# Optimization experiments

Measured on AMD Instinct MI355X. Metric: run time of the kernel, lower is better.

## Reference

```python
import jax, jax.numpy as jnp
import numpy as np
import math

B, S, E, H = 1, 4096, 1024, 16
D = E // H  # head_dim = 64

def setup_inputs() -> dict:
    key = jax.random.key(0)
    kx, kq, kk, kv, ko = jax.random.split(key, 5)
    sc = 1.0 / math.sqrt(E)
    return {
        "x": jax.random.normal(kx, (B, S, E), dtype=jnp.float32),
        "Wq": jax.random.normal(kq, (E, E), dtype=jnp.float32) * sc,
        "Wk": jax.random.normal(kk, (E, E), dtype=jnp.float32) * sc,
        "Wv": jax.random.normal(kv, (E, E), dtype=jnp.float32) * sc,
        "Wo": jax.random.normal(ko, (E, E), dtype=jnp.float32) * sc,
    }

def reference(x, Wq, Wk, Wv, Wo):
    b, s, _ = x.shape
    # nn.Linear(no bias): x @ W.T ; then split heads -> [b, H, s, D]
    def heads(w):
        return (x @ w.T).reshape(b, s, H, D).transpose(0, 2, 1, 3)
    q, k, v = heads(Wq), heads(Wk), heads(Wv)
    scale = 1.0 / math.sqrt(D)
    logits = jnp.einsum('bhqd,bhkd->bhqk', q, k) * scale  # [b,H,s,s]
    causal = jnp.tril(jnp.ones((s, s), dtype=bool))
    logits = jnp.where(causal, logits, -jnp.inf)
    attn = jax.nn.softmax(logits, axis=-1)
    out = jnp.einsum('bhqk,bhkd->bhqd', attn, v)  # [b,H,s,D]
    out = out.transpose(0, 2, 1, 3).reshape(b, s, E)
    return out @ Wo.T
```

## Files before the change

### kernel.cpp

```cpp
#include <hip/hip_runtime.h>
#include <hip/hip_bf16.h>

typedef unsigned short u16;
typedef unsigned int u32;
typedef __attribute__((ext_vector_type(8))) short short8;
typedef __attribute__((ext_vector_type(4))) float f32x4;
typedef __attribute__((ext_vector_type(16))) float f32x16;
typedef __attribute__((ext_vector_type(4))) u32 u32x4;
typedef __attribute__((ext_vector_type(2))) u32 u32x2;


__device__ __forceinline__ u16 f2b(float f) {
  unsigned u = __float_as_uint(f);
  u = (u + 0x7FFFu + ((u >> 16) & 1u)) >> 16;
  return (u16)u;
}

__device__ __forceinline__ u32 pkbf(float lo, float hi) {
  __hip_bfloat162 b = __float22bfloat162_rn(make_float2(lo, hi));
  u32 r;
  __builtin_memcpy(&r, &b, 4);
  return r;
}

__device__ __forceinline__ u32x2 plswap(u32 a, u32 b) {
  return __builtin_amdgcn_permlane32_swap(a, b, false, false);
}

__device__ __forceinline__ void gload16(const void* g, void* l) {
  __builtin_amdgcn_global_load_lds(
      (const __attribute__((address_space(1))) void*)g,
      (__attribute__((address_space(3))) void*)l, 16, 0, 0);
}


__global__ __launch_bounds__(256) void f2bf_kernel(const float* __restrict__ in,
                                                   u16* __restrict__ out, int n,
                                                   float scale) {
  int i = (blockIdx.x * 256 + threadIdx.x) * 4;
  if (i >= n) return;
  float4 v = *(const float4*)(in + i);
  unsigned p0 = (unsigned)f2b(v.x * scale) | ((unsigned)f2b(v.y * scale) << 16);
  unsigned p1 = (unsigned)f2b(v.z * scale) | ((unsigned)f2b(v.w * scale) << 16);
  *(uint2*)(out + i) = make_uint2(p0, p1);
}

__global__ __launch_bounds__(256) void f2bf4_kernel(
    const float* __restrict__ w0, const float* __restrict__ w1,
    const float* __restrict__ w2, const float* __restrict__ w3,
    u16* __restrict__ o0, u16* __restrict__ o1, u16* __restrict__ o2,
    u16* __restrict__ o3, float scale0) {
  const int y = blockIdx.y;
  const float* in = (y == 0) ? w0 : (y == 1) ? w1 : (y == 2) ? w2 : w3;
  u16* out = (y == 0) ? o0 : (y == 1) ? o1 : (y == 2) ? o2 : o3;
  const float scale = (y == 0) ? scale0 : 1.f;
  int i = (blockIdx.x * 256 + threadIdx.x) * 4;
  float4 v = *(const float4*)(in + i);
  unsigned p0 = (unsigned)f2b(v.x * scale) | ((unsigned)f2b(v.y * scale) << 16);
  unsigned p1 = (unsigned)f2b(v.z * scale) | ((unsigned)f2b(v.w * scale) << 16);
  *(uint2*)(out + i) = make_uint2(p0, p1);
}


__global__ __launch_bounds__(256) void transpose_kernel(const u16* __restrict__ V,
                                                        u16* __restrict__ Vt) {
  __shared__ u16 t[32][33];
  int bx = blockIdx.x;
  int by = blockIdx.y;
  int c = threadIdx.x & 31, r4 = threadIdx.x >> 5;
#pragma unroll
  for (int i = 0; i < 4; ++i) {
    int row = r4 * 4 + i;
    t[row][c] = V[(size_t)(by * 32 + row) * 1024 + bx * 32 + c];
  }
  __syncthreads();
#pragma unroll
  for (int i = 0; i < 4; ++i) {
    int row = r4 * 4 + i;
    Vt[(size_t)(bx * 32 + row) * 4096 + by * 32 + c] = t[c][row];
  }
}


__device__ __forceinline__ void storeC(u16* C, size_t idx, float v) { C[idx] = f2b(v); }
__device__ __forceinline__ void storeC(float* C, size_t idx, float v) { C[idx] = v; }

template <int BN, typename OutT>
__device__ __forceinline__ void gemm_body(const u16* __restrict__ A,
                                          const u16* __restrict__ B,
                                          OutT* __restrict__ C) {
  constexpr int NF = BN / 32;
  constexpr int BJ = BN / 32;
  __shared__ __align__(16) u16 lA[128 * 64];
  __shared__ __align__(16) u16 lB[BN * 64];
  const int tid = threadIdx.x;
  const int w = tid >> 6, lane = tid & 63, g = lane >> 4, lr = lane & 15;
  const int wr = w >> 1, wc = w & 1;
  const int m0 = blockIdx.y * 128, n0 = blockIdx.x * BN;

  f32x4 acc[4][NF] = {};

  for (int k0 = 0; k0 < 1024; k0 += 64) {
#pragma unroll
    for (int j = 0; j < 4; ++j) {
      int c = tid + j * 256;
      int row = c >> 3, sub = (c & 7) ^ (row & 7);
      gload16(A + (size_t)(m0 + row) * 1024 + k0 + sub * 8,
              &lA[(j * 256 + w * 64) * 8]);
      if (j < BJ)
        gload16(B + (size_t)(n0 + row) * 1024 + k0 + sub * 8,
                &lB[(j * 256 + w * 64) * 8]);
    }
    __syncthreads();

#pragma unroll
    for (int k2 = 0; k2 < 2; ++k2) {
      short8 af[4], bf[NF];
#pragma unroll
      for (int i = 0; i < 4; ++i) {
        int row = wr * 64 + i * 16 + lr;
        af[i] = *(const short8*)&lA[row * 64 + ((((k2 << 2) | g) ^ (row & 7)) << 3)];
      }
#pragma unroll
      for (int i = 0; i < NF; ++i) {
        int row = wc * (BN / 2) + i * 16 + lr;
        bf[i] = *(const short8*)&lB[row * 64 + ((((k2 << 2) | g) ^ (row & 7)) << 3)];
      }
#pragma unroll
      for (int mi = 0; mi < 4; ++mi)
#pragma unroll
        for (int ni = 0; ni < NF; ++ni)
          acc[mi][ni] = __builtin_amdgcn_mfma_f32_16x16x32_bf16(af[mi], bf[ni],
                                                                acc[mi][ni], 0, 0, 0);
    }
    __syncthreads();
  }

#pragma unroll
  for (int mi = 0; mi < 4; ++mi)
#pragma unroll
    for (int ni = 0; ni < NF; ++ni)
#pragma unroll
      for (int r = 0; r < 4; ++r) {
        size_t row = (size_t)(m0 + wr * 64 + mi * 16 + g * 4 + r);
        size_t col = (size_t)(n0 + wc * (BN / 2) + ni * 16 + lr);
        storeC(C, row * 1024 + col, acc[mi][ni][r]);
      }
}

__global__ __launch_bounds__(256) void gemm_qkv_kernel(
    const u16* __restrict__ A, const u16* __restrict__ W0, const u16* __restrict__ W1,
    const u16* __restrict__ W2, u16* __restrict__ C0, u16* __restrict__ C1,
    u16* __restrict__ C2) {
  int z = blockIdx.z;
  const u16* B = (z == 0) ? W0 : (z == 1) ? W1 : W2;
  u16* C = (z == 0) ? C0 : (z == 1) ? C1 : C2;
  gemm_body<128, u16>(A, B, C);
}

__global__ __launch_bounds__(256) void gemm_out_kernel(const u16* __restrict__ A,
                                                       const u16* __restrict__ B,
                                                       float* __restrict__ C) {
  gemm_body<64, float>(A, B, C);
}


#define NEGINF (-30000.0f)

__global__ __launch_bounds__(512, 4) void attn_kernel(const u16* __restrict__ Qg,
                                                      const u16* __restrict__ Kg,
                                                      const u16* __restrict__ Vtg,
                                                      u16* __restrict__ Og) {
  __shared__ __align__(16) char smem[65536];
  __shared__ float lll[4][32];

  const int tid = threadIdx.x, lane = tid & 63;
  const int w8 = tid >> 6, p = w8 >> 2, qw = w8 & 3;
  const int l31 = lane & 31, hi = lane >> 5;
  const int bid = blockIdx.x;
  const int h = bid & 15;
  const int i32 = bid >> 4;
  const int qb = (i32 < 16) ? (31 - i32) : (i32 - 16);
  const int qs = qb * 128;
  const int qsw = qs + qw * 32;
  const int iters = qb + 1;
  const int kstart = p ? iters : 0;
  const int dtw = qsw >> 6;
  const int swz = (l31 & 7) << 4;

  const u32x4 onesu = {0x3F803F80u, 0x3F803F80u, 0x3F803F80u, 0x3F803F80u};
  const short8 ones = __builtin_bit_cast(short8, onesu);

  short8 qf[4];
  {
    const u16* Qp = Qg + (size_t)(qsw + l31) * 1024 + h * 64 + hi * 8;
#pragma unroll
    for (int kc = 0; kc < 4; ++kc) qf[kc] = *(const short8*)(Qp + kc * 16);
  }

  const int j0 = qw * 2;
  auto stage = [&](int b, int kt) {
    char* Kb = smem + (((p << 1) | b) << 14);
    char* Vb = Kb + 8192;
#pragma unroll
    for (int jj = 0; jj < 2; ++jj) {
      const int j = j0 + jj;
      const int row = (j << 3) + (lane >> 3);
      const int c = (lane & 7) ^ (row & 7);
      gload16(Kg + (size_t)(kt * 64 + row) * 1024 + h * 64 + c * 8,
              Kb + (j << 10));
      gload16(Vtg + (size_t)(h * 64 + row) * 4096 + kt * 64 + c * 8,
              Vb + (j << 10));
    }
  };

  f32x16 ot[2] = {};
  f32x16 lacc = {};

  int cur = 0;
  stage(0, kstart);
  __syncthreads();

  for (int it = 0; it < iters; ++it) {
    const int kt = kstart + it;
    if (it + 1 < iters) stage(cur ^ 1, kt + 1);

    const bool doCompute = (p == 0) || (kt <= dtw);
    if (doCompute) {
      const char* Kb = smem + (((p << 1) | cur) << 14);
      const char* Vb = Kb + 8192;

      f32x16 st0 = {}, st1 = {};
#pragma unroll
      for (int kc = 0; kc < 4; ++kc) {
        short8 k0 = *(const short8*)(Kb + l31 * 128 + ((((kc << 1) | hi) << 4) ^ swz));
        st0 = __builtin_amdgcn_mfma_f32_32x32x16_bf16(k0, qf[kc], st0, 0, 0, 0);
      }
#pragma unroll
      for (int kc = 0; kc < 4; ++kc) {
        short8 k1 =
            *(const short8*)(Kb + 4096 + l31 * 128 + ((((kc << 1) | hi) << 4) ^ swz));
        st1 = __builtin_amdgcn_mfma_f32_32x32x16_bf16(k1, qf[kc], st1, 0, 0, 0);
      }

      if (kt == dtw) {
        const int q = qsw + l31;
#pragma unroll
        for (int r = 0; r < 16; ++r) {
          int key = kt * 64 + (r & 3) + 8 * (r >> 2) + 4 * hi;
          if (key > q) st0[r] = NEGINF;
          if (key + 32 > q) st1[r] = NEGINF;
        }
      }

#pragma unroll
      for (int r = 0; r < 16; ++r) {
        st0[r] = __builtin_amdgcn_exp2f(st0[r] - 12.f);
        st1[r] = __builtin_amdgcn_exp2f(st1[r] - 12.f);
      }

#pragma unroll
      for (int kt2 = 0; kt2 < 2; ++kt2) {
        const f32x16& st = kt2 ? st1 : st0;
        short8 pa[2];
#pragma unroll
        for (int ks = 0; ks < 2; ++ks) {
          const int b = 8 * ks;
          u32 pk0 = pkbf(st[b + 0], st[b + 1]);
          u32 pk1 = pkbf(st[b + 2], st[b + 3]);
          u32 pk2 = pkbf(st[b + 4], st[b + 5]);
          u32 pk3 = pkbf(st[b + 6], st[b + 7]);
          u32x2 r02 = plswap(pk0, pk2);
          u32x2 r13 = plswap(pk1, pk3);
          u32x4 t;
          t.x = r02.x;
          t.y = r13.x;
          t.z = r02.y;
          t.w = r13.y;
          pa[ks] = __builtin_bit_cast(short8, t);
        }
        lacc = __builtin_amdgcn_mfma_f32_32x32x16_bf16(ones, pa[0], lacc, 0, 0, 0);
        lacc = __builtin_amdgcn_mfma_f32_32x32x16_bf16(ones, pa[1], lacc, 0, 0, 0);
#pragma unroll
        for (int dt = 0; dt < 2; ++dt)
#pragma unroll
          for (int ks = 0; ks < 2; ++ks) {
            short8 vfv = *(const short8*)(Vb + dt * 4096 + l31 * 128 +
                                          (((kt2 * 4 + ks * 2 + hi) << 4) ^ swz));
            ot[dt] =
                __builtin_amdgcn_mfma_f32_32x32x16_bf16(vfv, pa[ks], ot[dt], 0, 0, 0);
          }
      }
    }
    __syncthreads();
    cur ^= 1;
  }

  __syncthreads();
  float* lOfw = (float*)smem + (qw << 11);
  char* pw = smem + 32768 + (qw << 12);
  if (p == 0) {
#pragma unroll
    for (int dt = 0; dt < 2; ++dt)
#pragma unroll
      for (int r = 0; r < 16; ++r) {
        int d = dt * 32 + (r & 3) + 8 * (r >> 2) + 4 * hi;
        lOfw[d * 32 + l31] = ot[dt][r];
      }
    if (hi == 0) lll[qw][l31] = lacc[0];
  }
  __syncthreads();
  if (p == 1) {
    float inv = 1.0f / (lll[qw][l31] + lacc[0]);
#pragma unroll
    for (int dt = 0; dt < 2; ++dt)
#pragma unroll
      for (int r = 0; r < 16; ++r) {
        int d = dt * 32 + (r & 3) + 8 * (r >> 2) + 4 * hi;
        float val = (lOfw[d * 32 + l31] + ot[dt][r]) * inv;
        *(u16*)(pw + l31 * 128 + ((d * 2) ^ ((l31 & 7) << 4))) = f2b(val);
      }
  }
  __syncthreads();
  if (p == 1) {
    const int row = lane >> 1;
#pragma unroll
    for (int ii = 0; ii < 4; ++ii) {
      int c = (lane & 1) * 4 + ii;
      short8 v = *(const short8*)(pw + row * 128 + ((c * 16) ^ ((row & 7) << 4)));
      *(short8*)(Og + (size_t)(qsw + row) * 1024 + h * 64 + c * 8) = v;
    }
  }
}


extern "C" void kernel_launch(void* const* d_in, const int* in_sizes, int n_in,
                              void* d_out, int out_size, void* d_ws, size_t ws_size,
                              hipStream_t stream) {
  const float* x = (const float*)d_in[0];
  const float* Wq = (const float*)d_in[1];
  const float* Wk = (const float*)d_in[2];
  const float* Wv = (const float*)d_in[3];
  const float* Wo = (const float*)d_in[4];
  float* out = (float*)d_out;
  char* ws = (char*)d_ws;
  const size_t MB = 1024 * 1024;

  u16* xb  = (u16*)(ws);
  u16* wqb = (u16*)(ws + 8 * MB);
  u16* wkb = (u16*)(ws + 10 * MB);
  u16* wvb = (u16*)(ws + 12 * MB);
  u16* wob = (u16*)(ws + 14 * MB);
  u16* Qb  = (u16*)(ws + 16 * MB);
  u16* Kb  = (u16*)(ws + 24 * MB);
  u16* Vb  = (u16*)(ws + 32 * MB);
  u16* Vtb = (u16*)(ws + 40 * MB);
  u16* att = xb;

  const float qscale = 0.125f * 1.4426950408889634f;

  f2bf_kernel<<<4096, 256, 0, stream>>>(x, xb, 4096 * 1024, 1.f);
  f2bf4_kernel<<<dim3(1024, 4), 256, 0, stream>>>(Wq, Wk, Wv, Wo, wqb, wkb, wvb,
                                                  wob, qscale);

  gemm_qkv_kernel<<<dim3(8, 32, 3), 256, 0, stream>>>(xb, wqb, wkb, wvb, Qb, Kb, Vb);
  transpose_kernel<<<dim3(32, 128), 256, 0, stream>>>(Vb, Vtb);
  attn_kernel<<<512, 512, 0, stream>>>(Qb, Kb, Vtb, att);
  gemm_out_kernel<<<dim3(16, 32), 256, 0, stream>>>(att, wob, out);
}
```

Measured before the change: 134.0 us.

## Fuse V transpose into QKV GEMM epilogue and merge conversion kernels

The V projection GEMM now writes its output already transposed through an LDS staging buffer, which removes the separate transpose kernel and the extra round trip of V through global memory. The x and weight fp32-to-bf16 conversions are merged into one launch to cut launch overhead. The attention kernel moves its small lll array into the existing shared buffer to trim LDS use. The transposed epilogue adds a barrier and LDS traffic inside the GEMM.

```diff
diff --git a/kernel.cpp b/kernel.cpp
--- a/kernel.cpp
+++ b/kernel.cpp
@@ -34,65 +34,46 @@
 }
 
 
-__global__ __launch_bounds__(256) void f2bf_kernel(const float* __restrict__ in,
-                                                   u16* __restrict__ out, int n,
-                                                   float scale) {
-  int i = (blockIdx.x * 256 + threadIdx.x) * 4;
-  if (i >= n) return;
-  float4 v = *(const float4*)(in + i);
+__global__ __launch_bounds__(256) void cvt_all_kernel(
+    const float* __restrict__ x, const float* __restrict__ w0,
+    const float* __restrict__ w1, const float* __restrict__ w2,
+    const float* __restrict__ w3, u16* __restrict__ xo, u16* __restrict__ o0,
+    u16* __restrict__ o1, u16* __restrict__ o2, u16* __restrict__ o3,
+    float scale0) {
+  const int bid = blockIdx.x;
+  const float* in;
+  u16* out;
+  float scale = 1.f;
+  int i;
+  if (bid < 4096) {
+    in = x; out = xo; i = bid;
+  } else {
+    const int k = (bid - 4096) >> 10;
+    i = (bid - 4096) & 1023;
+    in = (k == 0) ? w0 : (k == 1) ? w1 : (k == 2) ? w2 : w3;
+    out = (k == 0) ? o0 : (k == 1) ? o1 : (k == 2) ? o2 : o3;
+    if (k == 0) scale = scale0;
+  }
+  int idx = (i * 256 + threadIdx.x) * 4;
+  float4 v = *(const float4*)(in + idx);
   unsigned p0 = (unsigned)f2b(v.x * scale) | ((unsigned)f2b(v.y * scale) << 16);
   unsigned p1 = (unsigned)f2b(v.z * scale) | ((unsigned)f2b(v.w * scale) << 16);
-  *(uint2*)(out + i) = make_uint2(p0, p1);
-}
-
-__global__ __launch_bounds__(256) void f2bf4_kernel(
-    const float* __restrict__ w0, const float* __restrict__ w1,
-    const float* __restrict__ w2, const float* __restrict__ w3,
-    u16* __restrict__ o0, u16* __restrict__ o1, u16* __restrict__ o2,
-    u16* __restrict__ o3, float scale0) {
-  const int y = blockIdx.y;
-  const float* in = (y == 0) ? w0 : (y == 1) ? w1 : (y == 2) ? w2 : w3;
-  u16* out = (y == 0) ? o0 : (y == 1) ? o1 : (y == 2) ? o2 : o3;
-  const float scale = (y == 0) ? scale0 : 1.f;
-  int i = (blockIdx.x * 256 + threadIdx.x) * 4;
-  float4 v = *(const float4*)(in + i);
-  unsigned p0 = (unsigned)f2b(v.x * scale) | ((unsigned)f2b(v.y * scale) << 16);
-  unsigned p1 = (unsigned)f2b(v.z * scale) | ((unsigned)f2b(v.w * scale) << 16);
-  *(uint2*)(out + i) = make_uint2(p0, p1);
-}
-
-
-__global__ __launch_bounds__(256) void transpose_kernel(const u16* __restrict__ V,
-                                                        u16* __restrict__ Vt) {
-  __shared__ u16 t[32][33];
-  int bx = blockIdx.x;
-  int by = blockIdx.y;
-  int c = threadIdx.x & 31, r4 = threadIdx.x >> 5;
-#pragma unroll
-  for (int i = 0; i < 4; ++i) {
-    int row = r4 * 4 + i;
-    t[row][c] = V[(size_t)(by * 32 + row) * 1024 + bx * 32 + c];
-  }
-  __syncthreads();
-#pragma unroll
-  for (int i = 0; i < 4; ++i) {
-    int row = r4 * 4 + i;
-    Vt[(size_t)(bx * 32 + row) * 4096 + by * 32 + c] = t[c][row];
-  }
+  *(uint2*)(out + idx) = make_uint2(p0, p1);
 }
 
 
 __device__ __forceinline__ void storeC(u16* C, size_t idx, float v) { C[idx] = f2b(v); }
 __device__ __forceinline__ void storeC(float* C, size_t idx, float v) { C[idx] = v; }
 
-template <int BN, typename OutT>
+template <int BN, bool VT, typename OutT>
 __device__ __forceinline__ void gemm_body(const u16* __restrict__ A,
                                           const u16* __restrict__ B,
                                           OutT* __restrict__ C) {
   constexpr int NF = BN / 32;
   constexpr int BJ = BN / 32;
-  __shared__ __align__(16) u16 lA[128 * 64];
-  __shared__ __align__(16) u16 lB[BN * 64];
+  __shared__ __align__(16) u16 lAB[(128 + BN) * 64];
+  u16* lA = lAB;
+  u16* lB = lAB + 128 * 64;
   const int tid = threadIdx.x;
   const int w = tid >> 6, lane = tid & 63, g = lane >> 4, lr = lane & 15;
   const int wr = w >> 1, wc = w & 1;
@@ -136,32 +117,60 @@
     __syncthreads();
   }
 
-#pragma unroll
-  for (int mi = 0; mi < 4; ++mi)
-#pragma unroll
-    for (int ni = 0; ni < NF; ++ni)
-#pragma unroll
-      for (int r = 0; r < 4; ++r) {
-        size_t row = (size_t)(m0 + wr * 64 + mi * 16 + g * 4 + r);
-        size_t col = (size_t)(n0 + wc * (BN / 2) + ni * 16 + lr);
-        storeC(C, row * 1024 + col, acc[mi][ni][r]);
-      }
+  if constexpr (VT) {
+    char* pw = (char*)lAB + (w << 13);
+#pragma unroll
+    for (int mi = 0; mi < 4; ++mi)
+#pragma unroll
+      for (int ni = 0; ni < NF; ++ni)
+#pragma unroll
+        for (int r = 0; r < 4; ++r) {
+          int trow = ni * 16 + lr;
+          int tcol = mi * 16 + g * 4 + r;
+          *(u16*)(pw + trow * 128 + ((tcol * 2) ^ ((trow & 7) << 4))) =
+              f2b(acc[mi][ni][r]);
+        }
+    __syncthreads();
+#pragma unroll
+    for (int pass = 0; pass < 8; ++pass) {
+      int row = pass * 8 + (lane >> 3);
+      int ck = lane & 7;
+      short8 v = *(const short8*)(pw + row * 128 + ((ck * 16) ^ ((row & 7) << 4)));
+      *(short8*)((u16*)C + (size_t)(n0 + wc * 64 + row) * 4096 + m0 + wr * 64 +
+                 ck * 8) = v;
+    }
+  } else {
+#pragma unroll
+    for (int mi = 0; mi < 4; ++mi)
+#pragma unroll
+      for (int ni = 0; ni < NF; ++ni)
+#pragma unroll
+        for (int r = 0; r < 4; ++r) {
+          size_t row = (size_t)(m0 + wr * 64 + mi * 16 + g * 4 + r);
+          size_t col = (size_t)(n0 + wc * (BN / 2) + ni * 16 + lr);
+          storeC(C, row * 1024 + col, acc[mi][ni][r]);
+        }
+  }
 }
 
 __global__ __launch_bounds__(256) void gemm_qkv_kernel(
     const u16* __restrict__ A, const u16* __restrict__ W0, const u16* __restrict__ W1,
     const u16* __restrict__ W2, u16* __restrict__ C0, u16* __restrict__ C1,
-    u16* __restrict__ C2) {
+    u16* __restrict__ Vt) {
   int z = blockIdx.z;
-  const u16* B = (z == 0) ? W0 : (z == 1) ? W1 : W2;
-  u16* C = (z == 0) ? C0 : (z == 1) ? C1 : C2;
-  gemm_body<128, u16>(A, B, C);
+  if (z == 2) {
+    gemm_body<128, true, u16>(A, W2, Vt);
+  } else {
+    const u16* B = (z == 0) ? W0 : W1;
+    u16* C = (z == 0) ? C0 : C1;
+    gemm_body<128, false, u16>(A, B, C);
+  }
 }
 
 __global__ __launch_bounds__(256) void gemm_out_kernel(const u16* __restrict__ A,
                                                        const u16* __restrict__ B,
                                                        float* __restrict__ C) {
-  gemm_body<64, float>(A, B, C);
+  gemm_body<64, false, float>(A, B, C);
 }
 
 
@@ -172,7 +181,6 @@
                                                       const u16* __restrict__ Vtg,
                                                       u16* __restrict__ Og) {
   __shared__ __align__(16) char smem[65536];
-  __shared__ float lll[4][32];
 
   const int tid = threadIdx.x, lane = tid & 63;
   const int w8 = tid >> 6, p = w8 >> 2, qw = w8 & 3;
@@ -299,6 +307,7 @@
   __syncthreads();
   float* lOfw = (float*)smem + (qw << 11);
   char* pw = smem + 32768 + (qw << 12);
+  float* lll = (float*)(smem + 49152) + (qw << 5);
   if (p == 0) {
 #pragma unroll
     for (int dt = 0; dt < 2; ++dt)
@@ -307,11 +316,11 @@
         int d = dt * 32 + (r & 3) + 8 * (r >> 2) + 4 * hi;
         lOfw[d * 32 + l31] = ot[dt][r];
       }
-    if (hi == 0) lll[qw][l31] = lacc[0];
+    if (hi == 0) lll[l31] = lacc[0];
   }
   __syncthreads();
   if (p == 1) {
-    float inv = 1.0f / (lll[qw][l31] + lacc[0]);
+    float inv = 1.0f / (lll[l31] + lacc[0]);
 #pragma unroll
     for (int dt = 0; dt < 2; ++dt)
 #pragma unroll
@@ -353,18 +362,16 @@
   u16* wob = (u16*)(ws + 14 * MB);
   u16* Qb  = (u16*)(ws + 16 * MB);
   u16* Kb  = (u16*)(ws + 24 * MB);
-  u16* Vb  = (u16*)(ws + 32 * MB);
-  u16* Vtb = (u16*)(ws + 40 * MB);
+  u16* Vtb = (u16*)(ws + 32 * MB);
   u16* att = xb;
 
   const float qscale = 0.125f * 1.4426950408889634f;
 
-  f2bf_kernel<<<4096, 256, 0, stream>>>(x, xb, 4096 * 1024, 1.f);
-  f2bf4_kernel<<<dim3(1024, 4), 256, 0, stream>>>(Wq, Wk, Wv, Wo, wqb, wkb, wvb,
-                                                  wob, qscale);
-
-  gemm_qkv_kernel<<<dim3(8, 32, 3), 256, 0, stream>>>(xb, wqb, wkb, wvb, Qb, Kb, Vb);
-  transpose_kernel<<<dim3(32, 128), 256, 0, stream>>>(Vb, Vtb);
+  cvt_all_kernel<<<8192, 256, 0, stream>>>(x, Wq, Wk, Wv, Wo, xb, wqb, wkb, wvb,
+                                           wob, qscale);
+
+  gemm_qkv_kernel<<<dim3(8, 32, 3), 256, 0, stream>>>(xb, wqb, wkb, wvb, Qb, Kb,
+                                                      Vtb);
   attn_kernel<<<512, 512, 0, stream>>>(Qb, Kb, Vtb, att);
   gemm_out_kernel<<<dim3(16, 32), 256, 0, stream>>>(att, wob, out);
 }
```

Result: slower. 137.1 us (+2.3%).
